# Kernel optimization log

Hardware: AMD Instinct MI355X
Metric: run time of the kernel (lower is better)

Reference implementation:

```python
import jax, jax.numpy as jnp
import numpy as np

LK = 8  # db4 has 8 taps
LEVEL = 5
# pywt.Wavelet('db4').filter_bank[0] == dec_lo
DB4_LO = np.array([-0.010597401784997278, 0.032883011666982945, 0.030841381835986965,
                   -0.18703481171888114, -0.02798376941698385, 0.6308807679295904,
                   0.7148465705525415, 0.23037781330885523], dtype=np.float32)
DN = ('NCH', 'OIH', 'NCH')


def _wpt_kernels(level):
    # Filter_Free WPT: distinct kernel per child node; parent j even -> (lp, hp), odd -> (hp, lp)
    cmf = (-1.0) ** np.arange(LK)
    k_lp = DB4_LO
    k_hp = (DB4_LO[::-1] * cmf).astype(np.float32)
    ks = []
    for i in range(level):
        rows = []
        for j in range(2 ** i):
            rows += [k_lp, k_hp] if j % 2 == 0 else [k_hp, k_lp]
        ks.append(jnp.asarray(np.stack(rows)))  # [2^(i+1), LK]
    return ks


def setup_inputs() -> dict:
    key = jax.random.key(0)
    kx, kb = jax.random.split(key)
    B, N = 128, 32768
    inp = {'x': jax.random.normal(kx, (B, 1, N), dtype=jnp.float32)}
    for i, K in enumerate(_wpt_kernels(LEVEL)):
        inp[f'k{i + 1}'] = K
    for i in range(LEVEL):
        kb, sub = jax.random.split(kb)
        # small positive thresholds (Act_Init=0 would make the threshold an exact identity)
        inp[f'b{i + 1}'] = 0.1 * jax.random.uniform(sub, (2 ** (i + 1),), dtype=jnp.float32)
    return inp


def _analysis(c, K, b):
    # c: [B, G, M] parents -> [B, 2G, M//2] children; one grouped 8-tap conv for the whole level
    G = c.shape[1]
    cp = jnp.pad(c, ((0, 0), (0, 0), (LK // 2 - 1, LK // 2)))
    y = jax.lax.conv_general_dilated(cp, K[:, None, :], (2,), 'VALID',
                                     feature_group_count=G, dimension_numbers=DN)
    bb = b[None, :, None]
    # symmetric sigmoid soft-threshold (Thresh_SigSym), fused elementwise
    return y * (jax.nn.sigmoid(10.0 * (y - bb)) + jax.nn.sigmoid(-10.0 * (y + bb)))


def _synthesis(y, K):
    # adjoint of the strided analysis conv (conv_transpose): [B, 2G, M] -> [B, G, 2M]
    G = y.shape[1] // 2
    M = y.shape[2]
    W = jnp.flip(K, -1).reshape(G, 2, LK)  # sum the two children of each parent
    out = jax.lax.conv_general_dilated(y, W, (1,), [(LK - 1, LK - 1)], lhs_dilation=(2,),
                                       feature_group_count=G, dimension_numbers=DN)
    pl = LK // 2 - 1  # undo analysis left pad
    return out[:, :, pl:pl + 2 * M]


def reference(x, k1, k2, k3, k4, k5, b1, b2, b3, b4, b5):
    Ks = [k1, k2, k3, k4, k5]
    bs = [b1, b2, b3, b4, b5]
    c = x  # [B, 1, N]
    for K, b in zip(Ks, bs):
        c = _analysis(c, K, b)
    for K in Ks[::-1]:
        c = _synthesis(c, K)
    return c  # [B, 1, N] reconstruction
```

## Files before the change

kernel.cpp:

```cpp
#include <hip/hip_runtime.h>

#define TPB 512

constexpr int NSEQ = 32768;
constexpr int C0   = 4096;
constexpr float SCG = 14.4269504089f;


typedef float f2 __attribute__((ext_vector_type(2)));

__device__ __forceinline__ f2 sp(float x) { return (f2){x, x}; }
__device__ __forceinline__ f2 fma2(f2 a, f2 b, f2 c) { return __builtin_elementwise_fma(a, b, c); }

__device__ __forceinline__ float4 ldf4(const float* p) { return *reinterpret_cast<const float4*>(p); }
__device__ __forceinline__ void   stf4(float* p, const float4 v) { *reinterpret_cast<float4*>(p) = v; }

__device__ __forceinline__ float rfl(float x) {
    return __builtin_bit_cast(float, __builtin_amdgcn_readfirstlane(__builtin_bit_cast(int, x)));
}

__device__ __forceinline__ f2 gated2(f2 y, f2 tb) {
    f2 t1 = fma2(y, sp(-SCG), tb);
    f2 t2 = fma2(y, sp( SCG), tb);
    f2 s;
    s[0] = __builtin_amdgcn_rcpf(1.f + __builtin_amdgcn_exp2f(t1[0]))
         + __builtin_amdgcn_rcpf(1.f + __builtin_amdgcn_exp2f(t2[0]));
    s[1] = __builtin_amdgcn_rcpf(1.f + __builtin_amdgcn_exp2f(t1[1]))
         + __builtin_amdgcn_rcpf(1.f + __builtin_amdgcn_exp2f(t2[1]));
    return y * s;
}

template<int LEin, int P, int PAIRS, int Nlev, bool EDGE, int OUTSTRIDE, int EOOFF, bool LAST = false>
__device__ __forceinline__ void analysis8(
    const float* __restrict__ in, float* __restrict__ out,
    const f2* __restrict__ klh, const float* __restrict__ bias, int outBase)
{
    constexpr int TPC = P / 8;
    constexpr int TOT = PAIRS * TPC;
    static_assert(TOT <= TPB, "analysis phase must be single-generation");
    const int task = threadIdx.x;
    if (task < TOT) {
        const int c  = task / TPC;
        const int i0 = (task - c * TPC) * 8;

        const float* pe = in + c * (2 * LEin) + i0;
        const float* po = pe + LEin;
        float a[12], b[12];
        reinterpret_cast<float4*>(a)[0] = ldf4(pe);
        reinterpret_cast<float4*>(a)[1] = ldf4(pe + 4);
        reinterpret_cast<float4*>(a)[2] = ldf4(pe + 8);
        reinterpret_cast<float4*>(b)[0] = ldf4(po);
        reinterpret_cast<float4*>(b)[1] = ldf4(po + 4);
        reinterpret_cast<float4*>(b)[2] = ldf4(po + 8);

        const int sw    = c & 1;
        const int ch_lp = 2 * c + sw;
        const int ch_hp = 2 * c + 1 - sw;
        const f2  tb    = (f2){bias[ch_lp], bias[ch_hp]};

        if (LAST) {
            f2 v[8];
#pragma unroll
            for (int r = 0; r < 8; ++r) {
                f2 y = (f2){0.f, 0.f};
#pragma unroll
                for (int u = 0; u < 4; ++u) {
                    y = fma2(sp(a[r + u]), klh[2 * u], y);
                    y = fma2(sp(b[r + u]), klh[2 * u + 1], y);
                }
                y = gated2(y, tb);
                if (EDGE) {
                    const bool ok = ((unsigned)(outBase + i0 + r) < (unsigned)Nlev);
                    y[0] = ok ? y[0] : 0.f;
                    y[1] = ok ? y[1] : 0.f;
                }
                v[r] = y;
            }
            float* ol = out + ch_lp * OUTSTRIDE + i0;
            float* oh = out + ch_hp * OUTSTRIDE + i0;
            stf4(ol,     make_float4(v[0][0], v[1][0], v[2][0], v[3][0]));
            stf4(ol + 4, make_float4(v[4][0], v[5][0], v[6][0], v[7][0]));
            stf4(oh,     make_float4(v[0][1], v[1][1], v[2][1], v[3][1]));
            stf4(oh + 4, make_float4(v[4][1], v[5][1], v[6][1], v[7][1]));
        } else {
            const int j0 = i0 >> 1;
            float* ol = out + ch_lp * OUTSTRIDE + j0;
            float* oh = out + ch_hp * OUTSTRIDE + j0;
#pragma unroll
            for (int par = 0; par < 2; ++par) {
                f2 w[4];
#pragma unroll
                for (int k = 0; k < 4; ++k) {
                    const int r = 2 * k + par;
                    f2 y = (f2){0.f, 0.f};
#pragma unroll
                    for (int u = 0; u < 4; ++u) {
                        y = fma2(sp(a[r + u]), klh[2 * u], y);
                        y = fma2(sp(b[r + u]), klh[2 * u + 1], y);
                    }
                    y = gated2(y, tb);
                    if (EDGE) {
                        const bool ok = ((unsigned)(outBase + i0 + 2 * k + par) < (unsigned)Nlev);
                        y[0] = ok ? y[0] : 0.f;
                        y[1] = ok ? y[1] : 0.f;
                    }
                    w[k] = y;
                }
                stf4(ol + par * EOOFF, make_float4(w[0][0], w[1][0], w[2][0], w[3][0]));
                stf4(oh + par * EOOFF, make_float4(w[0][1], w[1][1], w[2][1], w[3][1]));
            }
        }
    }
}

template<int JROFF, bool EDGE>
__device__ __forceinline__ void synth_core(
    const float* __restrict__ ya, const float* __restrict__ yb,
    const f2* __restrict__ lrev, const f2* __restrict__ hrev,
    int gpos, int Nlev, float* __restrict__ o)
{
    f2 p1 = (f2){0.f, 0.f}, p2 = (f2){0.f, 0.f}, p3 = (f2){0.f, 0.f};
    float o0 = 0.f, o7 = 0.f;
#pragma unroll
    for (int q = 0; q < 4; ++q) {
        const f2 cl = lrev[q], ch = hrev[q];
        o0 = fmaf(ya[JROFF + q],     cl[1], o0);
        o0 = fmaf(yb[JROFF + q],     ch[1], o0);
        o7 = fmaf(ya[JROFF + 4 + q], cl[0], o7);
        o7 = fmaf(yb[JROFF + 4 + q], ch[0], o7);
        p1 = fma2(sp(ya[JROFF + 1 + q]), cl, p1);
        p1 = fma2(sp(yb[JROFF + 1 + q]), ch, p1);
        p2 = fma2(sp(ya[JROFF + 2 + q]), cl, p2);
        p2 = fma2(sp(yb[JROFF + 2 + q]), ch, p2);
        p3 = fma2(sp(ya[JROFF + 3 + q]), cl, p3);
        p3 = fma2(sp(yb[JROFF + 3 + q]), ch, p3);
    }
    o[0] = o0;    o[1] = p1[0]; o[2] = p1[1]; o[3] = p2[0];
    o[4] = p2[1]; o[5] = p3[0]; o[6] = p3[1]; o[7] = o7;
    if (EDGE) {
#pragma unroll
        for (int r = 0; r < 8; ++r) {
            const bool ok = ((unsigned)(gpos + r) < (unsigned)Nlev);
            o[r] = ok ? o[r] : 0.f;
        }
    }
}

template<int INSTRIDE, int Sout, int G, int Nlev, bool EDGE>
__device__ __forceinline__ void synthN(
    const float* __restrict__ in, float* __restrict__ out,
    const f2* __restrict__ lrev, const f2* __restrict__ hrev, int outBase)
{
    constexpr int TPG = Sout / 8;
    constexpr int TOT = G * TPG;
    static_assert(TOT <= 2 * TPB, "synth phase must fit in two generations");
#pragma unroll
    for (int t = threadIdx.x; t < TOT; t += TPB) {
        const int g   = t / TPG;
        const int nl0 = (t - g * TPG) * 8;
        const int sw  = g & 1;

        const float* p0 = in + (2 * g + sw)     * INSTRIDE + nl0 / 2;
        const float* p1 = in + (2 * g + 1 - sw) * INSTRIDE + nl0 / 2;
        float ya[8], yb[8];
        reinterpret_cast<float4*>(ya)[0] = ldf4(p0);
        reinterpret_cast<float4*>(ya)[1] = ldf4(p0 + 4);
        reinterpret_cast<float4*>(yb)[0] = ldf4(p1);
        reinterpret_cast<float4*>(yb)[1] = ldf4(p1 + 4);

        float o[8];
        synth_core<0, EDGE>(ya, yb, lrev, hrev, outBase + nl0, Nlev, o);
        float* op = out + g * Sout + nl0;
        stf4(op,     make_float4(o[0], o[1], o[2], o[3]));
        stf4(op + 4, make_float4(o[4], o[5], o[6], o[7]));
    }
}

template<bool EDGE>
__device__ __forceinline__ void run_chunk(
    const float* __restrict__ xb, float* __restrict__ ob, int s,
    float* __restrict__ bufA, float* __restrict__ bufB,
    const f2* __restrict__ klh, const f2* __restrict__ lrev, const f2* __restrict__ hrev,
    const float* __restrict__ bss)
{
    const int tid = threadIdx.x;

    {
        const int base = s - 221;
        const int a0   = base - 3;
#pragma unroll
        for (int k = 0; k < 3; ++k) {
            const int q = tid + TPB * k;
            if (q < 1151) {
                const int a = a0 + 4 * q;
                float4 v;
                if (!EDGE || (a >= 0 && a + 3 < NSEQ)) {
                    v = ldf4(xb + a);
                } else {
                    v.x = ((unsigned)(a)     < (unsigned)NSEQ) ? xb[a]     : 0.f;
                    v.y = ((unsigned)(a + 1) < (unsigned)NSEQ) ? xb[a + 1] : 0.f;
                    v.z = ((unsigned)(a + 2) < (unsigned)NSEQ) ? xb[a + 2] : 0.f;
                    v.w = ((unsigned)(a + 3) < (unsigned)NSEQ) ? xb[a + 3] : 0.f;
                }
                const int jo = 2 * q - 2;
                const int je = 2 * q - 1;
                if ((unsigned)jo       < 2300u) bufA[2304 + jo]     = v.x;
                if ((unsigned)je       < 2300u) bufA[je]            = v.y;
                if ((unsigned)(jo + 1) < 2300u) bufA[2304 + jo + 1] = v.z;
                if ((unsigned)(je + 1) < 2300u) bufA[je + 1]        = v.w;
            }
        }
    }
    __syncthreads();

    analysis8<2304, 2296,  1, 16384, EDGE, 2296, 1148>(bufA, bufB, klh, bss + 0,  (s >> 1) - 109);
    __syncthreads();
    analysis8<1148, 1144,  2,  8192, EDGE, 1144,  572>(bufB, bufA, klh, bss + 2,  (s >> 2) - 53);
    __syncthreads();
    analysis8< 572,  568,  4,  4096, EDGE,  568,  284>(bufA, bufB, klh, bss + 6,  (s >> 3) - 25);
    __syncthreads();
    analysis8< 284,  280,  8,  2048, EDGE,  280,  140>(bufB, bufA, klh, bss + 14, (s >> 4) - 11);
    __syncthreads();
    analysis8< 140,  136, 16,  1024, EDGE,  136,    0, true>(bufA, bufB, klh, bss + 30, (s >> 5) - 4);
    __syncthreads();

    synthN< 136,  264, 16,  2048, EDGE>(bufB, bufA, lrev, hrev, (s >> 4) - 4);
    __syncthreads();
    synthN< 264,  520,  8,  4096, EDGE>(bufA, bufB, lrev, hrev, (s >> 3) - 4);
    __syncthreads();
    synthN< 520, 1032,  4,  8192, EDGE>(bufB, bufA, lrev, hrev, (s >> 2) - 4);
    __syncthreads();
    synthN<1032, 2056,  2, 16384, EDGE>(bufA, bufB, lrev, hrev, (s >> 1) - 4);
    __syncthreads();

    {
        const int i0 = tid * 8;
        float ya[12], yb[12];
        {
            const float* p0 = bufB + i0 / 2;
            const float* p1 = p0 + 2056;
            reinterpret_cast<float4*>(ya)[0] = ldf4(p0);
            reinterpret_cast<float4*>(ya)[1] = ldf4(p0 + 4);
            reinterpret_cast<float4*>(ya)[2] = ldf4(p0 + 8);
            reinterpret_cast<float4*>(yb)[0] = ldf4(p1);
            reinterpret_cast<float4*>(yb)[1] = ldf4(p1 + 4);
            reinterpret_cast<float4*>(yb)[2] = ldf4(p1 + 8);
        }
        float o[8];
        synth_core<2, false>(ya, yb, lrev, hrev, 0, 1 << 30, o);
        stf4(ob + i0,     make_float4(o[0], o[1], o[2], o[3]));
        stf4(ob + i0 + 4, make_float4(o[4], o[5], o[6], o[7]));
    }
}

__global__ __launch_bounds__(TPB, 8) void wpt_fused(
    const float* __restrict__ x,
    const float* __restrict__ K1, const float* __restrict__ K2,
    const float* __restrict__ K3, const float* __restrict__ K4,
    const float* __restrict__ K5,
    const float* __restrict__ B1, const float* __restrict__ B2,
    const float* __restrict__ B3, const float* __restrict__ B4,
    const float* __restrict__ B5,
    float* __restrict__ out)
{
    __shared__ __align__(16) float bufA[4608];
    __shared__ __align__(16) float bufB[4608];
    __shared__ float bss[62];

    const int tid   = threadIdx.x;
    const int batch = blockIdx.x >> 3;
    const int cid   = blockIdx.x & 7;
    const int s     = cid * C0;

    float lp[8], hp[8];
#pragma unroll
    for (int t = 0; t < 8; ++t) {
        lp[t] = rfl(K1[t]);
        hp[t] = rfl(K1[8 + t]);
    }
    f2 klh[8], lrev[4], hrev[4];
#pragma unroll
    for (int t = 0; t < 8; ++t) klh[t] = (f2){lp[t], hp[t]};
#pragma unroll
    for (int q = 0; q < 4; ++q) {
        lrev[q] = (f2){lp[6 - 2 * q], lp[7 - 2 * q]};
        hrev[q] = (f2){hp[6 - 2 * q], hp[7 - 2 * q]};
    }

    {
        const float* bin[5] = {B1, B2, B3, B4, B5};
        const int boff[5] = {0, 2, 6, 14, 30};
#pragma unroll
        for (int l = 0; l < 5; ++l)
            for (int i = tid; i < (2 << l); i += TPB) bss[boff[l] + i] = SCG * bin[l][i];
    }

    const float* xb = x + batch * NSEQ;
    float* ob = out + batch * NSEQ + s;

    if (cid == 0 || cid == 7)
        run_chunk<true >(xb, ob, s, bufA, bufB, klh, lrev, hrev, bss);
    else
        run_chunk<false>(xb, ob, s, bufA, bufB, klh, lrev, hrev, bss);
}

extern "C" void kernel_launch(void* const* d_in, const int* in_sizes, int n_in,
                              void* d_out, int out_size, void* d_ws, size_t ws_size,
                              hipStream_t stream) {
    const int nbatch = in_sizes[0] / NSEQ;
    wpt_fused<<<dim3(nbatch * (NSEQ / C0)), dim3(TPB), 0, stream>>>(
        (const float*)d_in[0],
        (const float*)d_in[1], (const float*)d_in[2],
        (const float*)d_in[3], (const float*)d_in[4],
        (const float*)d_in[5],
        (const float*)d_in[6], (const float*)d_in[7],
        (const float*)d_in[8], (const float*)d_in[9],
        (const float*)d_in[10],
        (float*)d_out);
}
```

Baseline: 111.9 us.

## Halve block size and give each thread two work items per phase

Cuts threads per block from 512 to 256 and has each thread handle two (or three) analysis/synthesis tasks. All shared-memory loads for a thread's tasks are issued before any compute, which raises instruction-level parallelism. Launch bounds change from 8 to 4 blocks per multiprocessor to match the smaller block. The likely aim is to spend fewer instructions on indexing per task and hide LDS latency better, at the cost of more registers per thread and fewer waves per block. Phases that used to fit in one pass now need two, and static asserts enforce that.

```diff
diff --git a/kernel.cpp b/kernel.cpp
--- a/kernel.cpp
+++ b/kernel.cpp
@@ -1,6 +1,6 @@
 #include <hip/hip_runtime.h>
 
-#define TPB 512
+#define TPB 256
 
 constexpr int NSEQ = 32768;
 constexpr int C0   = 4096;
@@ -14,6 +14,16 @@
 
 __device__ __forceinline__ float4 ldf4(const float* p) { return *reinterpret_cast<const float4*>(p); }
 __device__ __forceinline__ void   stf4(float* p, const float4 v) { *reinterpret_cast<float4*>(p) = v; }
+
+__device__ __forceinline__ void ld12(float* d, const float* p) {
+    reinterpret_cast<float4*>(d)[0] = ldf4(p);
+    reinterpret_cast<float4*>(d)[1] = ldf4(p + 4);
+    reinterpret_cast<float4*>(d)[2] = ldf4(p + 8);
+}
+__device__ __forceinline__ void ld8(float* d, const float* p) {
+    reinterpret_cast<float4*>(d)[0] = ldf4(p);
+    reinterpret_cast<float4*>(d)[1] = ldf4(p + 4);
+}
 
 __device__ __forceinline__ float rfl(float x) {
     return __builtin_bit_cast(float, __builtin_amdgcn_readfirstlane(__builtin_bit_cast(int, x)));
@@ -30,38 +40,51 @@
     return y * s;
 }
 
-template<int LEin, int P, int PAIRS, int Nlev, bool EDGE, int OUTSTRIDE, int EOOFF, bool LAST = false>
-__device__ __forceinline__ void analysis8(
-    const float* __restrict__ in, float* __restrict__ out,
-    const f2* __restrict__ klh, const float* __restrict__ bias, int outBase)
-{
-    constexpr int TPC = P / 8;
-    constexpr int TOT = PAIRS * TPC;
-    static_assert(TOT <= TPB, "analysis phase must be single-generation");
-    const int task = threadIdx.x;
-    if (task < TOT) {
-        const int c  = task / TPC;
-        const int i0 = (task - c * TPC) * 8;
-
-        const float* pe = in + c * (2 * LEin) + i0;
-        const float* po = pe + LEin;
-        float a[12], b[12];
-        reinterpret_cast<float4*>(a)[0] = ldf4(pe);
-        reinterpret_cast<float4*>(a)[1] = ldf4(pe + 4);
-        reinterpret_cast<float4*>(a)[2] = ldf4(pe + 8);
-        reinterpret_cast<float4*>(b)[0] = ldf4(po);
-        reinterpret_cast<float4*>(b)[1] = ldf4(po + 4);
-        reinterpret_cast<float4*>(b)[2] = ldf4(po + 8);
-
-        const int sw    = c & 1;
-        const int ch_lp = 2 * c + sw;
-        const int ch_hp = 2 * c + 1 - sw;
-        const f2  tb    = (f2){bias[ch_lp], bias[ch_hp]};
-
-        if (LAST) {
-            f2 v[8];
-#pragma unroll
-            for (int r = 0; r < 8; ++r) {
+template<int Nlev, bool EDGE, int OUTSTRIDE, int EOOFF, bool LAST>
+__device__ __forceinline__ void analysis_cs(
+    const float* __restrict__ a, const float* __restrict__ b, int c, int i0,
+    float* __restrict__ out, const f2* __restrict__ klh,
+    const float* __restrict__ bias, int outBase)
+{
+    const int sw    = c & 1;
+    const int ch_lp = 2 * c + sw;
+    const int ch_hp = 2 * c + 1 - sw;
+    const f2  tb    = (f2){bias[ch_lp], bias[ch_hp]};
+
+    if (LAST) {
+        f2 v[8];
+#pragma unroll
+        for (int r = 0; r < 8; ++r) {
+            f2 y = (f2){0.f, 0.f};
+#pragma unroll
+            for (int u = 0; u < 4; ++u) {
+                y = fma2(sp(a[r + u]), klh[2 * u], y);
+                y = fma2(sp(b[r + u]), klh[2 * u + 1], y);
+            }
+            y = gated2(y, tb);
+            if (EDGE) {
+                const bool ok = ((unsigned)(outBase + i0 + r) < (unsigned)Nlev);
+                y[0] = ok ? y[0] : 0.f;
+                y[1] = ok ? y[1] : 0.f;
+            }
+            v[r] = y;
+        }
+        float* ol = out + ch_lp * OUTSTRIDE + i0;
+        float* oh = out + ch_hp * OUTSTRIDE + i0;
+        stf4(ol,     make_float4(v[0][0], v[1][0], v[2][0], v[3][0]));
+        stf4(ol + 4, make_float4(v[4][0], v[5][0], v[6][0], v[7][0]));
+        stf4(oh,     make_float4(v[0][1], v[1][1], v[2][1], v[3][1]));
+        stf4(oh + 4, make_float4(v[4][1], v[5][1], v[6][1], v[7][1]));
+    } else {
+        const int j0 = i0 >> 1;
+        float* ol = out + ch_lp * OUTSTRIDE + j0;
+        float* oh = out + ch_hp * OUTSTRIDE + j0;
+#pragma unroll
+        for (int par = 0; par < 2; ++par) {
+            f2 w[4];
+#pragma unroll
+            for (int k = 0; k < 4; ++k) {
+                const int r = 2 * k + par;
                 f2 y = (f2){0.f, 0.f};
 #pragma unroll
                 for (int u = 0; u < 4; ++u) {
@@ -74,43 +97,43 @@
                     y[0] = ok ? y[0] : 0.f;
                     y[1] = ok ? y[1] : 0.f;
                 }
-                v[r] = y;
+                w[k] = y;
             }
-            float* ol = out + ch_lp * OUTSTRIDE + i0;
-            float* oh = out + ch_hp * OUTSTRIDE + i0;
-            stf4(ol,     make_float4(v[0][0], v[1][0], v[2][0], v[3][0]));
-            stf4(ol + 4, make_float4(v[4][0], v[5][0], v[6][0], v[7][0]));
-            stf4(oh,     make_float4(v[0][1], v[1][1], v[2][1], v[3][1]));
-            stf4(oh + 4, make_float4(v[4][1], v[5][1], v[6][1], v[7][1]));
-        } else {
-            const int j0 = i0 >> 1;
-            float* ol = out + ch_lp * OUTSTRIDE + j0;
-            float* oh = out + ch_hp * OUTSTRIDE + j0;
-#pragma unroll
-            for (int par = 0; par < 2; ++par) {
-                f2 w[4];
-#pragma unroll
-                for (int k = 0; k < 4; ++k) {
-                    const int r = 2 * k + par;
-                    f2 y = (f2){0.f, 0.f};
-#pragma unroll
-                    for (int u = 0; u < 4; ++u) {
-                        y = fma2(sp(a[r + u]), klh[2 * u], y);
-                        y = fma2(sp(b[r + u]), klh[2 * u + 1], y);
-                    }
-                    y = gated2(y, tb);
-                    if (EDGE) {
-                        const bool ok = ((unsigned)(outBase + i0 + 2 * k + par) < (unsigned)Nlev);
-                        y[0] = ok ? y[0] : 0.f;
-                        y[1] = ok ? y[1] : 0.f;
-                    }
-                    w[k] = y;
-                }
-                stf4(ol + par * EOOFF, make_float4(w[0][0], w[1][0], w[2][0], w[3][0]));
-                stf4(oh + par * EOOFF, make_float4(w[0][1], w[1][1], w[2][1], w[3][1]));
-            }
-        }
-    }
+            stf4(ol + par * EOOFF, make_float4(w[0][0], w[1][0], w[2][0], w[3][0]));
+            stf4(oh + par * EOOFF, make_float4(w[0][1], w[1][1], w[2][1], w[3][1]));
+        }
+    }
+}
+
+template<int LEin, int P, int PAIRS, int Nlev, bool EDGE, int OUTSTRIDE, int EOOFF, bool LAST = false>
+__device__ __forceinline__ void analysis8(
+    const float* __restrict__ in, float* __restrict__ out,
+    const f2* __restrict__ klh, const float* __restrict__ bias, int outBase)
+{
+    constexpr int TPC = P / 8;
+    constexpr int TOT = PAIRS * TPC;
+    static_assert(TOT > TPB && TOT <= 2 * TPB, "analysis must be dual-generation");
+    const int t0 = threadIdx.x;
+    const int t1 = t0 + TPB;
+    const bool has1 = (t1 < TOT);
+
+    const int c0 = t0 / TPC, i0 = (t0 - c0 * TPC) * 8;
+    const int c1 = t1 / TPC, i1 = (t1 - c1 * TPC) * 8;
+
+    float a0[12], b0[12], a1[12], b1[12];
+    {
+        const float* pe = in + c0 * (2 * LEin) + i0;
+        ld12(a0, pe);
+        ld12(b0, pe + LEin);
+    }
+    if (has1) {
+        const float* pe = in + c1 * (2 * LEin) + i1;
+        ld12(a1, pe);
+        ld12(b1, pe + LEin);
+    }
+    analysis_cs<Nlev, EDGE, OUTSTRIDE, EOOFF, LAST>(a0, b0, c0, i0, out, klh, bias, outBase);
+    if (has1)
+        analysis_cs<Nlev, EDGE, OUTSTRIDE, EOOFF, LAST>(a1, b1, c1, i1, out, klh, bias, outBase);
 }
 
 template<int JROFF, bool EDGE>
@@ -146,6 +169,19 @@
     }
 }
 
+template<int Sout, int Nlev, bool EDGE>
+__device__ __forceinline__ void synth_cs(
+    const float* __restrict__ ya, const float* __restrict__ yb, int g, int nl0,
+    float* __restrict__ out, const f2* __restrict__ lrev, const f2* __restrict__ hrev,
+    int outBase)
+{
+    float o[8];
+    synth_core<0, EDGE>(ya, yb, lrev, hrev, outBase + nl0, Nlev, o);
+    float* op = out + g * Sout + nl0;
+    stf4(op,     make_float4(o[0], o[1], o[2], o[3]));
+    stf4(op + 4, make_float4(o[4], o[5], o[6], o[7]));
+}
+
 template<int INSTRIDE, int Sout, int G, int Nlev, bool EDGE>
 __device__ __forceinline__ void synthN(
     const float* __restrict__ in, float* __restrict__ out,
@@ -153,26 +189,34 @@
 {
     constexpr int TPG = Sout / 8;
     constexpr int TOT = G * TPG;
-    static_assert(TOT <= 2 * TPB, "synth phase must fit in two generations");
-#pragma unroll
-    for (int t = threadIdx.x; t < TOT; t += TPB) {
-        const int g   = t / TPG;
-        const int nl0 = (t - g * TPG) * 8;
-        const int sw  = g & 1;
-
-        const float* p0 = in + (2 * g + sw)     * INSTRIDE + nl0 / 2;
-        const float* p1 = in + (2 * g + 1 - sw) * INSTRIDE + nl0 / 2;
-        float ya[8], yb[8];
-        reinterpret_cast<float4*>(ya)[0] = ldf4(p0);
-        reinterpret_cast<float4*>(ya)[1] = ldf4(p0 + 4);
-        reinterpret_cast<float4*>(yb)[0] = ldf4(p1);
-        reinterpret_cast<float4*>(yb)[1] = ldf4(p1 + 4);
-
-        float o[8];
-        synth_core<0, EDGE>(ya, yb, lrev, hrev, outBase + nl0, Nlev, o);
-        float* op = out + g * Sout + nl0;
-        stf4(op,     make_float4(o[0], o[1], o[2], o[3]));
-        stf4(op + 4, make_float4(o[4], o[5], o[6], o[7]));
+    static_assert(TOT >= 2 * TPB && TOT <= 3 * TPB, "synth: two full + tail");
+    const int t0 = threadIdx.x;
+    const int t1 = t0 + TPB;
+    const int g0 = t0 / TPG, nl00 = (t0 - g0 * TPG) * 8;
+    const int g1 = t1 / TPG, nl01 = (t1 - g1 * TPG) * 8;
+
+    float ya0[8], yb0[8], ya1[8], yb1[8];
+    {
+        const int sw = g0 & 1;
+        ld8(ya0, in + (2 * g0 + sw)     * INSTRIDE + nl00 / 2);
+        ld8(yb0, in + (2 * g0 + 1 - sw) * INSTRIDE + nl00 / 2);
+    }
+    {
+        const int sw = g1 & 1;
+        ld8(ya1, in + (2 * g1 + sw)     * INSTRIDE + nl01 / 2);
+        ld8(yb1, in + (2 * g1 + 1 - sw) * INSTRIDE + nl01 / 2);
+    }
+    synth_cs<Sout, Nlev, EDGE>(ya0, yb0, g0, nl00, out, lrev, hrev, outBase);
+    synth_cs<Sout, Nlev, EDGE>(ya1, yb1, g1, nl01, out, lrev, hrev, outBase);
+
+    const int t2 = t0 + 2 * TPB;
+    if (t2 < TOT) {
+        const int g2 = t2 / TPG, nl02 = (t2 - g2 * TPG) * 8;
+        const int sw = g2 & 1;
+        float ya2[8], yb2[8];
+        ld8(ya2, in + (2 * g2 + sw)     * INSTRIDE + nl02 / 2);
+        ld8(yb2, in + (2 * g2 + 1 - sw) * INSTRIDE + nl02 / 2);
+        synth_cs<Sout, Nlev, EDGE>(ya2, yb2, g2, nl02, out, lrev, hrev, outBase);
     }
 }
 
@@ -189,7 +233,7 @@
         const int base = s - 221;
         const int a0   = base - 3;
 #pragma unroll
-        for (int k = 0; k < 3; ++k) {
+        for (int k = 0; k < 5; ++k) {
             const int q = tid + TPB * k;
             if (q < 1151) {
                 const int a = a0 + 4 * q;
@@ -234,26 +278,23 @@
     __syncthreads();
 
     {
-        const int i0 = tid * 8;
-        float ya[12], yb[12];
-        {
+#pragma unroll
+        for (int k = 0; k < 2; ++k) {
+            const int t  = tid + TPB * k;
+            const int i0 = t * 8;
+            float ya[12], yb[12];
             const float* p0 = bufB + i0 / 2;
-            const float* p1 = p0 + 2056;
-            reinterpret_cast<float4*>(ya)[0] = ldf4(p0);
-            reinterpret_cast<float4*>(ya)[1] = ldf4(p0 + 4);
-            reinterpret_cast<float4*>(ya)[2] = ldf4(p0 + 8);
-            reinterpret_cast<float4*>(yb)[0] = ldf4(p1);
-            reinterpret_cast<float4*>(yb)[1] = ldf4(p1 + 4);
-            reinterpret_cast<float4*>(yb)[2] = ldf4(p1 + 8);
-        }
-        float o[8];
-        synth_core<2, false>(ya, yb, lrev, hrev, 0, 1 << 30, o);
-        stf4(ob + i0,     make_float4(o[0], o[1], o[2], o[3]));
-        stf4(ob + i0 + 4, make_float4(o[4], o[5], o[6], o[7]));
-    }
-}
-
-__global__ __launch_bounds__(TPB, 8) void wpt_fused(
+            ld12(ya, p0);
+            ld12(yb, p0 + 2056);
+            float o[8];
+            synth_core<2, false>(ya, yb, lrev, hrev, 0, 1 << 30, o);
+            stf4(ob + i0,     make_float4(o[0], o[1], o[2], o[3]));
+            stf4(ob + i0 + 4, make_float4(o[4], o[5], o[6], o[7]));
+        }
+    }
+}
+
+__global__ __launch_bounds__(TPB, 4) void wpt_fused(
     const float* __restrict__ x,
     const float* __restrict__ K1, const float* __restrict__ K2,
     const float* __restrict__ K3, const float* __restrict__ K4,
```

Result: no change. 111.1 us (-0.7%).

## Process two chunks per block with staggered stages to overlap independent work

Applied to the files above, without the earlier changes.

Each block now handles two adjacent chunks, offset by one stage, so every barrier-separated phase carries work from both chunks. This interleaves independent loads and compute to hide LDS latency and idle threads between stages, and halves the number of barriers per chunk. In exchange, shared memory per block doubles, the launch bound drops to 4 blocks per SM, register pressure rises and the grid shrinks to 512 blocks, which may reduce occupancy and load balance.

```diff
diff --git a/kernel.cpp b/kernel.cpp
--- a/kernel.cpp
+++ b/kernel.cpp
@@ -14,6 +14,16 @@
 
 __device__ __forceinline__ float4 ldf4(const float* p) { return *reinterpret_cast<const float4*>(p); }
 __device__ __forceinline__ void   stf4(float* p, const float4 v) { *reinterpret_cast<float4*>(p) = v; }
+
+__device__ __forceinline__ void ld12(float* d, const float* p) {
+    reinterpret_cast<float4*>(d)[0] = ldf4(p);
+    reinterpret_cast<float4*>(d)[1] = ldf4(p + 4);
+    reinterpret_cast<float4*>(d)[2] = ldf4(p + 8);
+}
+__device__ __forceinline__ void ld8(float* d, const float* p) {
+    reinterpret_cast<float4*>(d)[0] = ldf4(p);
+    reinterpret_cast<float4*>(d)[1] = ldf4(p + 4);
+}
 
 __device__ __forceinline__ float rfl(float x) {
     return __builtin_bit_cast(float, __builtin_amdgcn_readfirstlane(__builtin_bit_cast(int, x)));
@@ -30,38 +40,61 @@
     return y * s;
 }
 
-template<int LEin, int P, int PAIRS, int Nlev, bool EDGE, int OUTSTRIDE, int EOOFF, bool LAST = false>
-__device__ __forceinline__ void analysis8(
-    const float* __restrict__ in, float* __restrict__ out,
-    const f2* __restrict__ klh, const float* __restrict__ bias, int outBase)
-{
-    constexpr int TPC = P / 8;
-    constexpr int TOT = PAIRS * TPC;
-    static_assert(TOT <= TPB, "analysis phase must be single-generation");
-    const int task = threadIdx.x;
-    if (task < TOT) {
-        const int c  = task / TPC;
-        const int i0 = (task - c * TPC) * 8;
-
-        const float* pe = in + c * (2 * LEin) + i0;
-        const float* po = pe + LEin;
-        float a[12], b[12];
-        reinterpret_cast<float4*>(a)[0] = ldf4(pe);
-        reinterpret_cast<float4*>(a)[1] = ldf4(pe + 4);
-        reinterpret_cast<float4*>(a)[2] = ldf4(pe + 8);
-        reinterpret_cast<float4*>(b)[0] = ldf4(po);
-        reinterpret_cast<float4*>(b)[1] = ldf4(po + 4);
-        reinterpret_cast<float4*>(b)[2] = ldf4(po + 8);
-
-        const int sw    = c & 1;
-        const int ch_lp = 2 * c + sw;
-        const int ch_hp = 2 * c + 1 - sw;
-        const f2  tb    = (f2){bias[ch_lp], bias[ch_hp]};
-
-        if (LAST) {
-            f2 v[8];
-#pragma unroll
-            for (int r = 0; r < 8; ++r) {
+
+template<int LEin, int TPC>
+__device__ __forceinline__ void ana_ld(const float* in, int task, float* a, float* b) {
+    const int c  = task / TPC;
+    const int i0 = (task - c * TPC) * 8;
+    const float* pe = in + c * (2 * LEin) + i0;
+    ld12(a, pe);
+    ld12(b, pe + LEin);
+}
+
+template<int Nlev, bool EDGE, int OUTSTRIDE, int EOOFF, bool LAST>
+__device__ __forceinline__ void analysis_cs(
+    const float* __restrict__ a, const float* __restrict__ b, int c, int i0,
+    float* __restrict__ out, const f2* __restrict__ klh,
+    const float* __restrict__ bias, int outBase)
+{
+    const int sw    = c & 1;
+    const int ch_lp = 2 * c + sw;
+    const int ch_hp = 2 * c + 1 - sw;
+    const f2  tb    = (f2){bias[ch_lp], bias[ch_hp]};
+
+    if (LAST) {
+        f2 v[8];
+#pragma unroll
+        for (int r = 0; r < 8; ++r) {
+            f2 y = (f2){0.f, 0.f};
+#pragma unroll
+            for (int u = 0; u < 4; ++u) {
+                y = fma2(sp(a[r + u]), klh[2 * u], y);
+                y = fma2(sp(b[r + u]), klh[2 * u + 1], y);
+            }
+            y = gated2(y, tb);
+            if (EDGE) {
+                const bool ok = ((unsigned)(outBase + i0 + r) < (unsigned)Nlev);
+                y[0] = ok ? y[0] : 0.f;
+                y[1] = ok ? y[1] : 0.f;
+            }
+            v[r] = y;
+        }
+        float* ol = out + ch_lp * OUTSTRIDE + i0;
+        float* oh = out + ch_hp * OUTSTRIDE + i0;
+        stf4(ol,     make_float4(v[0][0], v[1][0], v[2][0], v[3][0]));
+        stf4(ol + 4, make_float4(v[4][0], v[5][0], v[6][0], v[7][0]));
+        stf4(oh,     make_float4(v[0][1], v[1][1], v[2][1], v[3][1]));
+        stf4(oh + 4, make_float4(v[4][1], v[5][1], v[6][1], v[7][1]));
+    } else {
+        const int j0 = i0 >> 1;
+        float* ol = out + ch_lp * OUTSTRIDE + j0;
+        float* oh = out + ch_hp * OUTSTRIDE + j0;
+#pragma unroll
+        for (int par = 0; par < 2; ++par) {
+            f2 w[4];
+#pragma unroll
+            for (int k = 0; k < 4; ++k) {
+                const int r = 2 * k + par;
                 f2 y = (f2){0.f, 0.f};
 #pragma unroll
                 for (int u = 0; u < 4; ++u) {
@@ -74,43 +107,30 @@
                     y[0] = ok ? y[0] : 0.f;
                     y[1] = ok ? y[1] : 0.f;
                 }
-                v[r] = y;
+                w[k] = y;
             }
-            float* ol = out + ch_lp * OUTSTRIDE + i0;
-            float* oh = out + ch_hp * OUTSTRIDE + i0;
-            stf4(ol,     make_float4(v[0][0], v[1][0], v[2][0], v[3][0]));
-            stf4(ol + 4, make_float4(v[4][0], v[5][0], v[6][0], v[7][0]));
-            stf4(oh,     make_float4(v[0][1], v[1][1], v[2][1], v[3][1]));
-            stf4(oh + 4, make_float4(v[4][1], v[5][1], v[6][1], v[7][1]));
-        } else {
-            const int j0 = i0 >> 1;
-            float* ol = out + ch_lp * OUTSTRIDE + j0;
-            float* oh = out + ch_hp * OUTSTRIDE + j0;
-#pragma unroll
-            for (int par = 0; par < 2; ++par) {
-                f2 w[4];
-#pragma unroll
-                for (int k = 0; k < 4; ++k) {
-                    const int r = 2 * k + par;
-                    f2 y = (f2){0.f, 0.f};
-#pragma unroll
-                    for (int u = 0; u < 4; ++u) {
-                        y = fma2(sp(a[r + u]), klh[2 * u], y);
-                        y = fma2(sp(b[r + u]), klh[2 * u + 1], y);
-                    }
-                    y = gated2(y, tb);
-                    if (EDGE) {
-                        const bool ok = ((unsigned)(outBase + i0 + 2 * k + par) < (unsigned)Nlev);
-                        y[0] = ok ? y[0] : 0.f;
-                        y[1] = ok ? y[1] : 0.f;
-                    }
-                    w[k] = y;
-                }
-                stf4(ol + par * EOOFF, make_float4(w[0][0], w[1][0], w[2][0], w[3][0]));
-                stf4(oh + par * EOOFF, make_float4(w[0][1], w[1][1], w[2][1], w[3][1]));
-            }
+            stf4(ol + par * EOOFF, make_float4(w[0][0], w[1][0], w[2][0], w[3][0]));
+            stf4(oh + par * EOOFF, make_float4(w[0][1], w[1][1], w[2][1], w[3][1]));
         }
     }
+}
+
+template<int TPC, int Nlev, bool EDGE, int OS, int EO, bool LAST>
+__device__ __forceinline__ void ana_do(const float* a, const float* b, int task,
+    float* out, const f2* klh, const float* bias, int outBase)
+{
+    const int c  = task / TPC;
+    const int i0 = (task - c * TPC) * 8;
+    analysis_cs<Nlev, EDGE, OS, EO, LAST>(a, b, c, i0, out, klh, bias, outBase);
+}
+
+template<int INSTRIDE, int TPG>
+__device__ __forceinline__ void syn_ld(const float* in, int task, float* ya, float* yb) {
+    const int g   = task / TPG;
+    const int nl0 = (task - g * TPG) * 8;
+    const int sw  = g & 1;
+    ld8(ya, in + (2 * g + sw)     * INSTRIDE + nl0 / 2);
+    ld8(yb, in + (2 * g + 1 - sw) * INSTRIDE + nl0 / 2);
 }
 
 template<int JROFF, bool EDGE>
@@ -146,106 +166,233 @@
     }
 }
 
-template<int INSTRIDE, int Sout, int G, int Nlev, bool EDGE>
-__device__ __forceinline__ void synthN(
-    const float* __restrict__ in, float* __restrict__ out,
-    const f2* __restrict__ lrev, const f2* __restrict__ hrev, int outBase)
-{
-    constexpr int TPG = Sout / 8;
-    constexpr int TOT = G * TPG;
-    static_assert(TOT <= 2 * TPB, "synth phase must fit in two generations");
-#pragma unroll
-    for (int t = threadIdx.x; t < TOT; t += TPB) {
-        const int g   = t / TPG;
-        const int nl0 = (t - g * TPG) * 8;
-        const int sw  = g & 1;
-
-        const float* p0 = in + (2 * g + sw)     * INSTRIDE + nl0 / 2;
-        const float* p1 = in + (2 * g + 1 - sw) * INSTRIDE + nl0 / 2;
-        float ya[8], yb[8];
-        reinterpret_cast<float4*>(ya)[0] = ldf4(p0);
-        reinterpret_cast<float4*>(ya)[1] = ldf4(p0 + 4);
-        reinterpret_cast<float4*>(yb)[0] = ldf4(p1);
-        reinterpret_cast<float4*>(yb)[1] = ldf4(p1 + 4);
-
-        float o[8];
-        synth_core<0, EDGE>(ya, yb, lrev, hrev, outBase + nl0, Nlev, o);
-        float* op = out + g * Sout + nl0;
-        stf4(op,     make_float4(o[0], o[1], o[2], o[3]));
-        stf4(op + 4, make_float4(o[4], o[5], o[6], o[7]));
-    }
+template<int TPG, int Sout, int Nlev, bool EDGE>
+__device__ __forceinline__ void syn_do(const float* ya, const float* yb, int task,
+    float* out, const f2* lrev, const f2* hrev, int outBase)
+{
+    const int g   = task / TPG;
+    const int nl0 = (task - g * TPG) * 8;
+    float o[8];
+    synth_core<0, EDGE>(ya, yb, lrev, hrev, outBase + nl0, Nlev, o);
+    float* op = out + g * Sout + nl0;
+    stf4(op,     make_float4(o[0], o[1], o[2], o[3]));
+    stf4(op + 4, make_float4(o[4], o[5], o[6], o[7]));
 }
 
 template<bool EDGE>
-__device__ __forceinline__ void run_chunk(
-    const float* __restrict__ xb, float* __restrict__ ob, int s,
-    float* __restrict__ bufA, float* __restrict__ bufB,
-    const f2* __restrict__ klh, const f2* __restrict__ lrev, const f2* __restrict__ hrev,
-    const float* __restrict__ bss)
-{
-    const int tid = threadIdx.x;
-
-    {
-        const int base = s - 221;
-        const int a0   = base - 3;
-#pragma unroll
-        for (int k = 0; k < 3; ++k) {
-            const int q = tid + TPB * k;
-            if (q < 1151) {
-                const int a = a0 + 4 * q;
-                float4 v;
-                if (!EDGE || (a >= 0 && a + 3 < NSEQ)) {
-                    v = ldf4(xb + a);
-                } else {
-                    v.x = ((unsigned)(a)     < (unsigned)NSEQ) ? xb[a]     : 0.f;
-                    v.y = ((unsigned)(a + 1) < (unsigned)NSEQ) ? xb[a + 1] : 0.f;
-                    v.z = ((unsigned)(a + 2) < (unsigned)NSEQ) ? xb[a + 2] : 0.f;
-                    v.w = ((unsigned)(a + 3) < (unsigned)NSEQ) ? xb[a + 3] : 0.f;
-                }
-                const int jo = 2 * q - 2;
-                const int je = 2 * q - 1;
-                if ((unsigned)jo       < 2300u) bufA[2304 + jo]     = v.x;
-                if ((unsigned)je       < 2300u) bufA[je]            = v.y;
-                if ((unsigned)(jo + 1) < 2300u) bufA[2304 + jo + 1] = v.z;
-                if ((unsigned)(je + 1) < 2300u) bufA[je + 1]        = v.w;
+__device__ __forceinline__ void stage_ld(const float* __restrict__ xb, int s, float4* v) {
+    const int tid = threadIdx.x;
+    const int a0  = s - 224;
+#pragma unroll
+    for (int k = 0; k < 3; ++k) {
+        const int q = tid + TPB * k;
+        float4 t = make_float4(0.f, 0.f, 0.f, 0.f);
+        if (q < 1151) {
+            const int a = a0 + 4 * q;
+            if (!EDGE || (a >= 0 && a + 3 < NSEQ)) {
+                t = ldf4(xb + a);
+            } else {
+                t.x = ((unsigned)(a)     < (unsigned)NSEQ) ? xb[a]     : 0.f;
+                t.y = ((unsigned)(a + 1) < (unsigned)NSEQ) ? xb[a + 1] : 0.f;
+                t.z = ((unsigned)(a + 2) < (unsigned)NSEQ) ? xb[a + 2] : 0.f;
+                t.w = ((unsigned)(a + 3) < (unsigned)NSEQ) ? xb[a + 3] : 0.f;
             }
         }
-    }
-    __syncthreads();
-
-    analysis8<2304, 2296,  1, 16384, EDGE, 2296, 1148>(bufA, bufB, klh, bss + 0,  (s >> 1) - 109);
-    __syncthreads();
-    analysis8<1148, 1144,  2,  8192, EDGE, 1144,  572>(bufB, bufA, klh, bss + 2,  (s >> 2) - 53);
-    __syncthreads();
-    analysis8< 572,  568,  4,  4096, EDGE,  568,  284>(bufA, bufB, klh, bss + 6,  (s >> 3) - 25);
-    __syncthreads();
-    analysis8< 284,  280,  8,  2048, EDGE,  280,  140>(bufB, bufA, klh, bss + 14, (s >> 4) - 11);
-    __syncthreads();
-    analysis8< 140,  136, 16,  1024, EDGE,  136,    0, true>(bufA, bufB, klh, bss + 30, (s >> 5) - 4);
-    __syncthreads();
-
-    synthN< 136,  264, 16,  2048, EDGE>(bufB, bufA, lrev, hrev, (s >> 4) - 4);
-    __syncthreads();
-    synthN< 264,  520,  8,  4096, EDGE>(bufA, bufB, lrev, hrev, (s >> 3) - 4);
-    __syncthreads();
-    synthN< 520, 1032,  4,  8192, EDGE>(bufB, bufA, lrev, hrev, (s >> 2) - 4);
-    __syncthreads();
-    synthN<1032, 2056,  2, 16384, EDGE>(bufA, bufB, lrev, hrev, (s >> 1) - 4);
-    __syncthreads();
+        v[k] = t;
+    }
+}
+__device__ __forceinline__ void stage_st(const float4* v, float* __restrict__ buf) {
+    const int tid = threadIdx.x;
+#pragma unroll
+    for (int k = 0; k < 3; ++k) {
+        const int q = tid + TPB * k;
+        if (q < 1151) {
+            const int jo = 2 * q - 2;
+            const int je = 2 * q - 1;
+            if ((unsigned)jo       < 2300u) buf[2304 + jo]     = v[k].x;
+            if ((unsigned)je       < 2300u) buf[je]            = v[k].y;
+            if ((unsigned)(jo + 1) < 2300u) buf[2304 + jo + 1] = v[k].z;
+            if ((unsigned)(je + 1) < 2300u) buf[je + 1]        = v[k].w;
+        }
+    }
+}
+
+
+template<int LA,int PA,int PRA,int NA,bool EA,int OSA,int EOA,bool LASTA,
+         int LB,int PB,int PRB,int NB,bool EB,int OSB,int EOB,bool LASTB>
+__device__ __forceinline__ void body_aa(
+    const float* Ain, float* Aout, const float* biasA, int obA,
+    const float* Bin, float* Bout, const float* biasB, int obB,
+    const f2* klh)
+{
+    const int tid = threadIdx.x;
+    constexpr int TPCA = PA / 8, TOTA = PRA * TPCA;
+    constexpr int TPCB = PB / 8, TOTB = PRB * TPCB;
+    const int tA = tid < TOTA ? tid : TOTA - 1;
+    const int tB = tid < TOTB ? tid : TOTB - 1;
+    float aA[12], bA[12], aB[12], bB[12];
+    ana_ld<LA, TPCA>(Ain, tA, aA, bA);
+    ana_ld<LB, TPCB>(Bin, tB, aB, bB);
+    if (tid < TOTA) ana_do<TPCA, NA, EA, OSA, EOA, LASTA>(aA, bA, tA, Aout, klh, biasA, obA);
+    if (tid < TOTB) ana_do<TPCB, NB, EB, OSB, EOB, LASTB>(aB, bB, tB, Bout, klh, biasB, obB);
+    __syncthreads();
+}
+
+template<int ISA,int SoA,int GA,int NA,bool EA,
+         int LB,int PB,int PRB,int NB,bool EB,int OSB,int EOB,bool LASTB>
+__device__ __forceinline__ void body_sa(
+    const float* Ain, float* Aout, int obA,
+    const float* Bin, float* Bout, const float* biasB, int obB,
+    const f2* klh, const f2* lrev, const f2* hrev)
+{
+    const int tid = threadIdx.x;
+    constexpr int TPGA = SoA / 8, TOTA = GA * TPGA;
+    constexpr int TPCB = PB / 8, TOTB = PRB * TPCB;
+    const int tB = tid < TOTB ? tid : TOTB - 1;
+    float yaA[8], ybA[8], aB[12], bB[12];
+    syn_ld<ISA, TPGA>(Ain, tid, yaA, ybA);
+    ana_ld<LB, TPCB>(Bin, tB, aB, bB);
+    syn_do<TPGA, SoA, NA, EA>(yaA, ybA, tid, Aout, lrev, hrev, obA);
+    if (tid < TOTB) ana_do<TPCB, NB, EB, OSB, EOB, LASTB>(aB, bB, tB, Bout, klh, biasB, obB);
+    if (tid + TPB < TOTA) {
+        const int t = tid + TPB;
+        float ya[8], yb[8];
+        syn_ld<ISA, TPGA>(Ain, t, ya, yb);
+        syn_do<TPGA, SoA, NA, EA>(ya, yb, t, Aout, lrev, hrev, obA);
+    }
+    __syncthreads();
+}
+
+template<int ISA,int SoA,int GA,int NA,bool EA,
+         int ISB,int SoB,int GB,int NB,bool EB>
+__device__ __forceinline__ void body_ss(
+    const float* Ain, float* Aout, int obA,
+    const float* Bin, float* Bout, int obB,
+    const f2* lrev, const f2* hrev)
+{
+    const int tid = threadIdx.x;
+    constexpr int TPGA = SoA / 8, TOTA = GA * TPGA;
+    constexpr int TPGB = SoB / 8, TOTB = GB * TPGB;
+    float yaA[8], ybA[8], yaB[8], ybB[8];
+    syn_ld<ISA, TPGA>(Ain, tid, yaA, ybA);
+    syn_ld<ISB, TPGB>(Bin, tid, yaB, ybB);
+    syn_do<TPGA, SoA, NA, EA>(yaA, ybA, tid, Aout, lrev, hrev, obA);
+    syn_do<TPGB, SoB, NB, EB>(yaB, ybB, tid, Bout, lrev, hrev, obB);
+    if (tid + TPB < TOTA) {
+        const int t = tid + TPB;
+        float ya[8], yb[8];
+        syn_ld<ISA, TPGA>(Ain, t, ya, yb);
+        syn_do<TPGA, SoA, NA, EA>(ya, yb, t, Aout, lrev, hrev, obA);
+    }
+    if (tid + TPB < TOTB) {
+        const int t = tid + TPB;
+        float ya[8], yb[8];
+        syn_ld<ISB, TPGB>(Bin, t, ya, yb);
+        syn_do<TPGB, SoB, NB, EB>(ya, yb, t, Bout, lrev, hrev, obB);
+    }
+    __syncthreads();
+}
+
+template<int ISB,int SoB,int GB,int NB,bool EB>
+__device__ __forceinline__ void body_fs(
+    const float* Afin, float* oa,
+    const float* Bin, float* Bout, int obB,
+    const f2* lrev, const f2* hrev)
+{
+    const int tid = threadIdx.x;
+    constexpr int TPGB = SoB / 8, TOTB = GB * TPGB;
+    const int i0 = tid * 8;
+    float ya[12], yb[12], yaB[8], ybB[8];
+    ld12(ya, Afin + i0 / 2);
+    ld12(yb, Afin + i0 / 2 + 2056);
+    syn_ld<ISB, TPGB>(Bin, tid, yaB, ybB);
+    {
+        float o[8];
+        synth_core<2, false>(ya, yb, lrev, hrev, 0, 1 << 30, o);
+        stf4(oa + i0,     make_float4(o[0], o[1], o[2], o[3]));
+        stf4(oa + i0 + 4, make_float4(o[4], o[5], o[6], o[7]));
+    }
+    syn_do<TPGB, SoB, NB, EB>(yaB, ybB, tid, Bout, lrev, hrev, obB);
+    if (tid + TPB < TOTB) {
+        const int t = tid + TPB;
+        float y2a[8], y2b[8];
+        syn_ld<ISB, TPGB>(Bin, t, y2a, y2b);
+        syn_do<TPGB, SoB, NB, EB>(y2a, y2b, t, Bout, lrev, hrev, obB);
+    }
+    __syncthreads();
+}
+
+
+template<bool EDGEA, bool EDGEB>
+__device__ __forceinline__ void run_pair(
+    const float* __restrict__ xb, float* __restrict__ oa, float* __restrict__ ob,
+    int sa, int sb,
+    float* A0, float* A1, float* B0, float* B1,
+    const f2* klh, const f2* lrev, const f2* hrev, const float* bss)
+{
+    const int tid = threadIdx.x;
+
+    {
+        float4 v[3];
+        stage_ld<EDGEA>(xb, sa, v);
+        stage_st(v, A0);
+    }
+    __syncthreads();
+
+    {
+        float4 v[3];
+        stage_ld<EDGEB>(xb, sb, v);
+        const int tA = tid < 287 ? tid : 286;
+        float a[12], b[12];
+        ana_ld<2304, 287>(A0, tA, a, b);
+        if (tid < 287)
+            ana_do<287, 16384, EDGEA, 2296, 1148, false>(a, b, tA, A1, klh, bss + 0, (sa >> 1) - 109);
+        stage_st(v, B0);
+    }
+    __syncthreads();
+
+    body_aa<1148,1144,2,8192,EDGEA,1144,572,false,
+            2304,2296,1,16384,EDGEB,2296,1148,false>(
+        A1, A0, bss + 2, (sa >> 2) - 53,
+        B0, B1, bss + 0, (sb >> 1) - 109, klh);
+
+    body_aa<572,568,4,4096,EDGEA,568,284,false,
+            1148,1144,2,8192,EDGEB,1144,572,false>(
+        A0, A1, bss + 6, (sa >> 3) - 25,
+        B1, B0, bss + 2, (sb >> 2) - 53, klh);
+
+    body_aa<284,280,8,2048,EDGEA,280,140,false,
+            572,568,4,4096,EDGEB,568,284,false>(
+        A1, A0, bss + 14, (sa >> 4) - 11,
+        B0, B1, bss + 6, (sb >> 3) - 25, klh);
+
+    body_aa<140,136,16,1024,EDGEA,136,0,true,
+            284,280,8,2048,EDGEB,280,140,false>(
+        A0, A1, bss + 30, (sa >> 5) - 4,
+        B1, B0, bss + 14, (sb >> 4) - 11, klh);
+
+    body_sa<136,264,16,2048,EDGEA,
+            140,136,16,1024,EDGEB,136,0,true>(
+        A1, A0, (sa >> 4) - 4,
+        B0, B1, bss + 30, (sb >> 5) - 4, klh, lrev, hrev);
+
+    body_ss<264,520,8,4096,EDGEA, 136,264,16,2048,EDGEB>(
+        A0, A1, (sa >> 3) - 4, B1, B0, (sb >> 4) - 4, lrev, hrev);
+
+    body_ss<520,1032,4,8192,EDGEA, 264,520,8,4096,EDGEB>(
+        A1, A0, (sa >> 2) - 4, B0, B1, (sb >> 3) - 4, lrev, hrev);
+
+    body_ss<1032,2056,2,16384,EDGEA, 520,1032,4,8192,EDGEB>(
+        A0, A1, (sa >> 1) - 4, B1, B0, (sb >> 2) - 4, lrev, hrev);
+
+    body_fs<1032,2056,2,16384,EDGEB>(
+        A1, oa, B0, B1, (sb >> 1) - 4, lrev, hrev);
 
     {
         const int i0 = tid * 8;
         float ya[12], yb[12];
-        {
-            const float* p0 = bufB + i0 / 2;
-            const float* p1 = p0 + 2056;
-            reinterpret_cast<float4*>(ya)[0] = ldf4(p0);
-            reinterpret_cast<float4*>(ya)[1] = ldf4(p0 + 4);
-            reinterpret_cast<float4*>(ya)[2] = ldf4(p0 + 8);
-            reinterpret_cast<float4*>(yb)[0] = ldf4(p1);
-            reinterpret_cast<float4*>(yb)[1] = ldf4(p1 + 4);
-            reinterpret_cast<float4*>(yb)[2] = ldf4(p1 + 8);
-        }
+        ld12(ya, B1 + i0 / 2);
+        ld12(yb, B1 + i0 / 2 + 2056);
         float o[8];
         synth_core<2, false>(ya, yb, lrev, hrev, 0, 1 << 30, o);
         stf4(ob + i0,     make_float4(o[0], o[1], o[2], o[3]));
@@ -253,7 +400,7 @@
     }
 }
 
-__global__ __launch_bounds__(TPB, 8) void wpt_fused(
+__global__ __launch_bounds__(TPB, 4) void wpt_fused(
     const float* __restrict__ x,
     const float* __restrict__ K1, const float* __restrict__ K2,
     const float* __restrict__ K3, const float* __restrict__ K4,
@@ -263,14 +410,17 @@
     const float* __restrict__ B5,
     float* __restrict__ out)
 {
-    __shared__ __align__(16) float bufA[4608];
-    __shared__ __align__(16) float bufB[4608];
+    __shared__ __align__(16) float A0[4608];
+    __shared__ __align__(16) float A1[4608];
+    __shared__ __align__(16) float Bb0[4608];
+    __shared__ __align__(16) float Bb1[4608];
     __shared__ float bss[62];
 
     const int tid   = threadIdx.x;
-    const int batch = blockIdx.x >> 3;
-    const int cid   = blockIdx.x & 7;
-    const int s     = cid * C0;
+    const int batch = blockIdx.x >> 2;
+    const int pair  = blockIdx.x & 3;
+    const int sa    = pair * (2 * C0);
+    const int sb    = sa + C0;
 
     float lp[8], hp[8];
 #pragma unroll
@@ -296,19 +446,22 @@
     }
 
     const float* xb = x + batch * NSEQ;
-    float* ob = out + batch * NSEQ + s;
-
-    if (cid == 0 || cid == 7)
-        run_chunk<true >(xb, ob, s, bufA, bufB, klh, lrev, hrev, bss);
+    float* oa = out + batch * NSEQ + sa;
+    float* ob = oa + C0;
+
+    if (pair == 0)
+        run_pair<true,  false>(xb, oa, ob, sa, sb, A0, A1, Bb0, Bb1, klh, lrev, hrev, bss);
+    else if (pair == 3)
+        run_pair<false, true >(xb, oa, ob, sa, sb, A0, A1, Bb0, Bb1, klh, lrev, hrev, bss);
     else
-        run_chunk<false>(xb, ob, s, bufA, bufB, klh, lrev, hrev, bss);
+        run_pair<false, false>(xb, oa, ob, sa, sb, A0, A1, Bb0, Bb1, klh, lrev, hrev, bss);
 }
 
 extern "C" void kernel_launch(void* const* d_in, const int* in_sizes, int n_in,
                               void* d_out, int out_size, void* d_ws, size_t ws_size,
                               hipStream_t stream) {
     const int nbatch = in_sizes[0] / NSEQ;
-    wpt_fused<<<dim3(nbatch * (NSEQ / C0)), dim3(TPB), 0, stream>>>(
+    wpt_fused<<<dim3(nbatch * 4), dim3(TPB), 0, stream>>>(
         (const float*)d_in[0],
         (const float*)d_in[1], (const float*)d_in[2],
         (const float*)d_in[3], (const float*)d_in[4],
```

Result: slower. 117.7 us (+5.1%).
